# Optimization experiments

Hardware: AMD Instinct MI355X
Metric: run time of the kernel (lower is better)

Reference implementation:

```python
import jax, jax.numpy as jnp
import numpy as np

B, C, H, W = 4, 512, 64, 64
C8 = C // 8
BN_EPS = 1e-5


def setup_inputs() -> dict:
    key = jax.random.key(0)
    ks = jax.random.split(key, 9)
    x = jax.random.normal(ks[0], (B, C, H, W), jnp.float32)
    # 1x1 convs are channel-mixing matrices (out_ch, in_ch), no bias
    wq = 0.02 * jax.random.normal(ks[1], (C8, C), jnp.float32)
    wk = 0.02 * jax.random.normal(ks[2], (C8, C), jnp.float32)
    wv = 0.02 * jax.random.normal(ks[3], (C, C), jnp.float32)
    w_fuse = 0.02 * jax.random.normal(ks[4], (C, C), jnp.float32)
    # gammas init to 0 in the module; use small random values so the
    # attention branches actually contribute to outputs/grads
    gamma_pa = 0.5 + 0.1 * jax.random.normal(ks[5], (1,), jnp.float32)
    gamma_ca = 0.5 + 0.1 * jax.random.normal(ks[6], (1,), jnp.float32)
    bn_scale = 1.0 + 0.1 * jax.random.normal(ks[7], (C,), jnp.float32)
    bn_bias = 0.1 * jax.random.normal(ks[8], (C,), jnp.float32)
    return {"x": x, "wq": wq, "wk": wk, "wv": wv, "w_fuse": w_fuse,
            "gamma_pa": gamma_pa, "gamma_ca": gamma_ca,
            "bn_scale": bn_scale, "bn_bias": bn_bias}


def reference(x, wq, wk, wv, w_fuse, gamma_pa, gamma_ca, bn_scale, bn_bias):
    b, c, h, w = x.shape
    n = h * w
    xf = x.reshape(b, c, n)                         # [B, C, N]

    # ---- Position attention (over N = H*W spatial positions) ----
    q = jnp.einsum('oc,bcn->bon', wq, xf)           # [B, C/8, N]
    k = jnp.einsum('oc,bcn->bon', wk, xf)           # [B, C/8, N]
    v = jnp.einsum('oc,bcn->bon', wv, xf)           # [B, C, N]
    energy = jnp.einsum('bcn,bcm->bnm', q, k)       # [B, N, N] (no scaling, as in source)
    attn = jax.nn.softmax(energy, axis=-1)
    # out = v @ attn^T  ->  out[b,c,n] = sum_m v[b,c,m] * attn[b,n,m]
    pa = jnp.einsum('bcm,bnm->bcn', v, attn).reshape(b, c, h, w)
    pa = gamma_pa * pa + x

    # ---- Channel attention (over C channels, max-subtracted variant) ----
    ce = jnp.einsum('bcn,bdn->bcd', xf, xf)         # [B, C, C]
    ce = jnp.max(ce, axis=-1, keepdims=True) - ce
    cattn = jax.nn.softmax(ce, axis=-1)
    ca = jnp.einsum('bcd,bdn->bcn', cattn, xf).reshape(b, c, h, w)
    ca = gamma_ca * ca + x

    # ---- Fuse: 1x1 conv -> BatchNorm (training-mode batch stats) -> ReLU ----
    s = pa + ca
    y = jnp.einsum('oc,bchw->bohw', w_fuse, s)
    mean = jnp.mean(y, axis=(0, 2, 3), keepdims=True)
    var = jnp.var(y, axis=(0, 2, 3), keepdims=True)
    y = (y - mean) * jax.lax.rsqrt(var + BN_EPS)
    y = y * bn_scale.reshape(1, -1, 1, 1) + bn_bias.reshape(1, -1, 1, 1)
    return jax.nn.relu(y)
```

## Files before the change

### kernel.cpp

```cpp
#include <hip/hip_runtime.h>
#include <cstdint>
#include <cstddef>

#define B_   4
#define C_   512
#define N_   4096
#define BN_EPS 1e-5f

typedef __attribute__((ext_vector_type(8))) short short8;
typedef __attribute__((ext_vector_type(8))) unsigned short ushort8;
typedef __attribute__((ext_vector_type(4))) unsigned short us4_t;
typedef __attribute__((ext_vector_type(4))) float f32x4;

__device__ __forceinline__ unsigned short f2b(float f) {
  union { float f; unsigned u; } v; v.f = f;
  unsigned u = v.u;
  return (unsigned short)((u + 0x7fffu + ((u >> 16) & 1u)) >> 16);
}
__device__ __forceinline__ float b2f(unsigned short h) {
  union { unsigned u; float f; } v; v.u = ((unsigned)h) << 16;
  return v.f;
}
__device__ __forceinline__ void async16(const void* g, void* l) {
  __builtin_amdgcn_global_load_lds((const __attribute__((address_space(1))) void*)g,
                                   (__attribute__((address_space(3))) void*)l, 16, 0, 0);
}


__global__ __launch_bounds__(256) void convert_x_k(const float* __restrict__ x,
                                                   unsigned short* __restrict__ xcn,
                                                   unsigned short* __restrict__ xnc) {
  __shared__ float tile[64][65];
  int c0 = blockIdx.x * 64, n0 = blockIdx.y * 64, b = blockIdx.z;
  const float* xb = x + ((size_t)b * C_ + c0) * N_ + n0;
  unsigned short* cn = xcn + ((size_t)b * C_ + c0) * N_ + n0;
#pragma unroll
  for (int j = 0; j < 16; ++j) {
    int lin = j * 256 + threadIdx.x;
    int rr = lin >> 6, cc = lin & 63;
    float v = xb[(size_t)rr * N_ + cc];
    cn[(size_t)rr * N_ + cc] = f2b(v);
    tile[cc][rr] = v;
  }
  __syncthreads();
  unsigned short* nc = xnc + ((size_t)b * N_ + n0) * C_ + c0;
#pragma unroll
  for (int j = 0; j < 16; ++j) {
    int lin = j * 256 + threadIdx.x;
    int rr = lin >> 6, cc = lin & 63;
    nc[(size_t)rr * C_ + cc] = f2b(tile[rr][cc]);
  }
}

__global__ __launch_bounds__(256) void convert_w_k(const float* __restrict__ wq, const float* __restrict__ wk,
                                                   const float* __restrict__ wv, const float* __restrict__ wf,
                                                   unsigned short* __restrict__ wqk,
                                                   unsigned short* __restrict__ wvb,
                                                   unsigned short* __restrict__ wfb) {
  int i = blockIdx.x * 256 + threadIdx.x;
  if (i < 128 * 512) {
    int row = i >> 9, col = i & 511;
    float v = (row < 64) ? wq[row * 512 + col] : wk[(row - 64) * 512 + col];
    wqk[i] = f2b(v);
  }
  wvb[i] = f2b(wv[i]);
  wfb[i] = f2b(wf[i]);
}


enum { EPI_BF16 = 0, EPI_F32 = 1 };

template<int EPI, bool SPLITK = false>
__global__ __launch_bounds__(256)
void gemm_bt(const unsigned short* __restrict__ A, size_t lda, size_t sA,
             const unsigned short* __restrict__ Bm, size_t ldb, size_t sB,
             void* __restrict__ Cv, size_t ldc, size_t sCbytes, int K) {
  const int bz = blockIdx.z;
  const int m0 = blockIdx.x * 128, n0 = blockIdx.y * 128;
  char* Cb;
  if (SPLITK) {
    int bidx = bz & 3, ch = bz >> 2;
    A  += (size_t)bidx * sA + (size_t)ch * (size_t)K;
    Bm += (size_t)bidx * sB + (size_t)ch * (size_t)K;
    Cb = (char*)Cv + (size_t)bidx * sCbytes + (size_t)ch * 4u * sCbytes;
  } else {
    A  += (size_t)bz * sA;
    Bm += (size_t)bz * sB;
    Cb = (char*)Cv + (size_t)bz * sCbytes;
  }
  __shared__ unsigned short lsA[128 * 32];
  __shared__ unsigned short lsB[128 * 32];
  const int tid = threadIdx.x, lane = tid & 63, w = tid >> 6;
  const int wm = (w >> 1) * 64, wn = (w & 1) * 64;
  const int fr = lane & 15, fk = (lane >> 4) * 8;
  f32x4 acc[4][4];
#pragma unroll
  for (int i = 0; i < 4; ++i)
#pragma unroll
    for (int j = 0; j < 4; ++j) acc[i][j] = (f32x4){0.f, 0.f, 0.f, 0.f};

  const int i0 = tid, i1 = tid + 256;
  for (int k0 = 0; k0 < K; k0 += 32) {
    async16(A  + (size_t)(m0 + (i0 >> 2)) * lda + k0 + (i0 & 3) * 8, (char*)lsA + i0 * 16);
    async16(A  + (size_t)(m0 + (i1 >> 2)) * lda + k0 + (i1 & 3) * 8, (char*)lsA + i1 * 16);
    async16(Bm + (size_t)(n0 + (i0 >> 2)) * ldb + k0 + (i0 & 3) * 8, (char*)lsB + i0 * 16);
    async16(Bm + (size_t)(n0 + (i1 >> 2)) * ldb + k0 + (i1 & 3) * 8, (char*)lsB + i1 * 16);
    __syncthreads();
    short8 af[4], bfr[4];
#pragma unroll
    for (int mi = 0; mi < 4; ++mi)
      af[mi] = *(const short8*)&lsA[(wm + mi * 16 + fr) * 32 + fk];
#pragma unroll
    for (int ni = 0; ni < 4; ++ni)
      bfr[ni] = *(const short8*)&lsB[(wn + ni * 16 + fr) * 32 + fk];
#pragma unroll
    for (int mi = 0; mi < 4; ++mi)
#pragma unroll
      for (int ni = 0; ni < 4; ++ni)
        acc[mi][ni] = __builtin_amdgcn_mfma_f32_16x16x32_bf16(af[mi], bfr[ni], acc[mi][ni], 0, 0, 0);
    __syncthreads();
  }
#pragma unroll
  for (int mi = 0; mi < 4; ++mi)
#pragma unroll
    for (int ni = 0; ni < 4; ++ni)
#pragma unroll
      for (int r = 0; r < 4; ++r) {
        int gr = m0 + wm + mi * 16 + (lane >> 4) * 4 + r;
        int gc = n0 + wn + ni * 16 + fr;
        float v = acc[mi][ni][r];
        if (EPI == EPI_BF16) ((unsigned short*)Cb)[(size_t)gr * ldc + gc] = f2b(v);
        else                 ((float*)Cb)[(size_t)gr * ldc + gc] = v;
      }
}

#define QR 128
#define CC 256
#define KT 128

__global__ __launch_bounds__(512, 2)
void fused_pa_k(const unsigned short* __restrict__ qkT,
                const unsigned short* __restrict__ vmat,
                const unsigned short* __restrict__ caT,
                const unsigned short* __restrict__ xnc,
                const float* __restrict__ gpa_p, const float* __restrict__ gca_p,
                unsigned short* __restrict__ sT) {
  __shared__ unsigned short lsQ[QR * 64];
  __shared__ unsigned short lsK[2][KT * 64];
  __shared__ unsigned short lsV[CC * KT];
  __shared__ unsigned short lsP[QR * KT];
  __shared__ float lsL[8][QR];
  __shared__ float invL[QR];

  const int bid = blockIdx.x;
  const int combo = bid & 7;
  const int b = combo >> 1, chalf = combo & 1;
  const int qt = bid >> 3;
  const int n0 = qt * QR, c0 = chalf * CC;

  const int tid = threadIdx.x, lane = tid & 63, w = tid >> 6;
  const int fr = lane & 15, fq = lane >> 4;
  const int wr = w >> 2, wc = w & 3;

  const unsigned short* qk_b = qkT + (size_t)b * N_ * 128;
  const unsigned short* v_b  = vmat + (size_t)b * C_ * N_;

  f32x4 acc[4][4];
#pragma unroll
  for (int i = 0; i < 4; ++i)
#pragma unroll
    for (int j = 0; j < 4; ++j) acc[i][j] = (f32x4){0.f, 0.f, 0.f, 0.f};
  float lsum[8];
#pragma unroll
  for (int f = 0; f < 8; ++f) lsum[f] = 0.f;

#pragma unroll
  for (int j = 0; j < 2; ++j) {
    int idx = j * 512 + tid;
    int r = idx >> 3, g = idx & 7;
    async16(qk_b + (size_t)(n0 + r) * 128 + ((g ^ (r & 7)) << 3), (char*)lsQ + idx * 16);
  }
#pragma unroll
  for (int j = 0; j < 2; ++j) {
    int idx = j * 512 + tid;
    int r = idx >> 3, g = idx & 7;
    async16(qk_b + (size_t)r * 128 + 64 + ((g ^ (r & 7)) << 3), (char*)lsK[0] + idx * 16);
  }
  __syncthreads();

  for (int it = 0; it < N_ / KT; ++it) {
    const int m0 = it * KT;
#pragma unroll
    for (int j = 0; j < 8; ++j) {
      int idx = j * 512 + tid;
      int c = idx >> 4, g = idx & 15;
      async16(v_b + (size_t)(c0 + c) * N_ + m0 + ((g ^ (c & 7)) << 3), (char*)lsV + idx * 16);
    }
    if (it < N_ / KT - 1) {
      unsigned short* dst = lsK[(it + 1) & 1];
#pragma unroll
      for (int j = 0; j < 2; ++j) {
        int idx = j * 512 + tid;
        int r = idx >> 3, g = idx & 7;
        async16(qk_b + (size_t)(m0 + KT + r) * 128 + 64 + ((g ^ (r & 7)) << 3),
                (char*)dst + idx * 16);
      }
    }
    const unsigned short* lk = lsK[it & 1];
    const int ms = w * 16;
    short8 afk[2];
#pragma unroll
    for (int kk = 0; kk < 2; ++kk)
      afk[kk] = *(const short8*)&lk[(ms + fr) * 64 + (((kk * 4 + fq) ^ (fr & 7)) << 3)];
#pragma unroll
    for (int f = 0; f < 8; ++f) {
      f32x4 e = (f32x4){0.f, 0.f, 0.f, 0.f};
#pragma unroll
      for (int kk = 0; kk < 2; ++kk) {
        short8 bq = *(const short8*)&lsQ[(f * 16 + fr) * 64 + (((kk * 4 + fq) ^ (fr & 7)) << 3)];
        e = __builtin_amdgcn_mfma_f32_16x16x32_bf16(afk[kk], bq, e, 0, 0, 0);
      }
      float p0 = __expf(e[0]), p1 = __expf(e[1]), p2 = __expf(e[2]), p3 = __expf(e[3]);
      float part = (p0 + p1) + (p2 + p3);
      part += __shfl_xor(part, 16, 64);
      part += __shfl_xor(part, 32, 64);
      lsum[f] += part;
      int n = f * 16 + fr;
      int mb = ms + fq * 4;
      us4_t pk = { f2b(p0), f2b(p1), f2b(p2), f2b(p3) };
      *(us4_t*)((char*)lsP + n * 256 + ((((mb >> 3) ^ (n & 7)) << 3) + (mb & 7)) * 2) = pk;
    }
    __syncthreads();
#pragma unroll
    for (int kk4 = 0; kk4 < 4; ++kk4) {
      short8 pa[4], vbf[4];
#pragma unroll
      for (int mi = 0; mi < 4; ++mi) {
        int n = wr * 64 + mi * 16 + fr;
        pa[mi] = *(const short8*)((const char*)lsP + n * 256 + (((kk4 * 4 + fq) ^ (n & 7)) << 4));
      }
#pragma unroll
      for (int ni = 0; ni < 4; ++ni) {
        int c = wc * 64 + ni * 16 + fr;
        vbf[ni] = *(const short8*)((const char*)lsV + c * 256 + (((kk4 * 4 + fq) ^ (c & 7)) << 4));
      }
#pragma unroll
      for (int mi = 0; mi < 4; ++mi)
#pragma unroll
        for (int ni = 0; ni < 4; ++ni)
          acc[mi][ni] = __builtin_amdgcn_mfma_f32_16x16x32_bf16(pa[mi], vbf[ni], acc[mi][ni], 0, 0, 0);
    }
    __syncthreads();
  }

  if (lane < 16) {
#pragma unroll
    for (int f = 0; f < 8; ++f) lsL[w][f * 16 + lane] = lsum[f];
  }
  __syncthreads();
  if (tid < QR) {
    float s = 0.f;
#pragma unroll
    for (int ww = 0; ww < 8; ++ww) s += lsL[ww][tid];
    invL[tid] = 1.f / s;
  }
  __syncthreads();

  const float gpa = gpa_p[0], gca = gca_p[0];
#pragma unroll
  for (int mi = 0; mi < 4; ++mi)
#pragma unroll
    for (int ni = 0; ni < 4; ++ni)
#pragma unroll
      for (int r = 0; r < 4; ++r) {
        int nl = wr * 64 + mi * 16 + fq * 4 + r;
        int gn = n0 + nl;
        int gc = c0 + wc * 64 + ni * 16 + fr;
        size_t eo = ((size_t)b * N_ + gn) * C_ + gc;
        float sv = gpa * acc[mi][ni][r] * invL[nl] + gca * b2f(caT[eo]) + 2.f * b2f(xnc[eo]);
        sT[eo] = f2b(sv);
      }
}

__global__ __launch_bounds__(256) void ce_softmax_k(const float* __restrict__ cepart,
                                                    unsigned short* __restrict__ cattn) {
  int wid = threadIdx.x >> 6, lane = threadIdx.x & 63;
  size_t row = (size_t)blockIdx.x * 4 + wid;
  float v[8]; float mn = 3.4e38f;
#pragma unroll
  for (int i = 0; i < 8; ++i) {
    size_t idx = row * C_ + (size_t)(i * 64 + lane);
    float t = cepart[idx] + cepart[idx + 1048576] + cepart[idx + 2097152] + cepart[idx + 3145728];
    v[i] = t; mn = fminf(mn, t);
  }
#pragma unroll
  for (int o = 1; o < 64; o <<= 1) mn = fminf(mn, __shfl_xor(mn, o, 64));
  float s = 0.f, p[8];
#pragma unroll
  for (int i = 0; i < 8; ++i) { p[i] = expf(mn - v[i]); s += p[i]; }
#pragma unroll
  for (int o = 1; o < 64; o <<= 1) s += __shfl_xor(s, o, 64);
  float inv = 1.f / s;
  unsigned short* orow = cattn + row * C_;
#pragma unroll
  for (int i = 0; i < 8; ++i) orow[i * 64 + lane] = f2b(p[i] * inv);
}

__global__ __launch_bounds__(256) void bn_part_k(const unsigned short* __restrict__ yT,
                                                 float* __restrict__ part) {
  int p = blockIdx.x, t = threadIdx.x;
  const unsigned short* base = yT + (size_t)p * 256 * C_;
  float s0 = 0, q0 = 0, s1 = 0, q1 = 0;
  for (int r = 0; r < 256; ++r) {
    float a = b2f(base[(size_t)r * C_ + t]);
    float b = b2f(base[(size_t)r * C_ + t + 256]);
    s0 += a; q0 += a * a; s1 += b; q1 += b * b;
  }
  float* pp = part + (size_t)p * 1024;
  pp[t] = s0; pp[t + 256] = s1; pp[t + 512] = q0; pp[t + 768] = q1;
}

__global__ __launch_bounds__(256) void bn_final_k(const float* __restrict__ part,
                                                  const float* __restrict__ bns,
                                                  const float* __restrict__ bnb,
                                                  float* __restrict__ ab) {
  int t = threadIdx.x;
#pragma unroll
  for (int cc = 0; cc < 2; ++cc) {
    int c = t + cc * 256;
    float s = 0, q = 0;
    for (int p = 0; p < 64; ++p) { s += part[p * 1024 + c]; q += part[p * 1024 + 512 + c]; }
    float mean = s * (1.f / 16384.f);
    float var  = q * (1.f / 16384.f) - mean * mean;
    float istd = rsqrtf(var + BN_EPS);
    float a = bns[c] * istd;
    float b = bnb[c] - mean * a;
    ab[c * 2] = a; ab[c * 2 + 1] = b;
  }
}

__global__ __launch_bounds__(256) void bn_apply_k(const unsigned short* __restrict__ yT,
                                                  const float* __restrict__ ab,
                                                  float* __restrict__ out) {
  __shared__ float tile[64][65];
  int n0 = blockIdx.x * 64, o0 = blockIdx.y * 64, b = blockIdx.z;
  const unsigned short* yb = yT + ((size_t)b * N_ + n0) * C_ + o0;
#pragma unroll
  for (int j = 0; j < 16; ++j) {
    int lin = j * 256 + threadIdx.x;
    int rr = lin >> 6, cc = lin & 63;
    float v = b2f(yb[(size_t)rr * C_ + cc]);
    float a = ab[(o0 + cc) * 2], bb = ab[(o0 + cc) * 2 + 1];
    tile[cc][rr] = fmaxf(v * a + bb, 0.f);
  }
  __syncthreads();
  float* ob = out + ((size_t)b * C_ + o0) * N_ + n0;
#pragma unroll
  for (int j = 0; j < 16; ++j) {
    int lin = j * 256 + threadIdx.x;
    int rr = lin >> 6, cc = lin & 63;
    ob[(size_t)rr * N_ + cc] = tile[rr][cc];
  }
}


extern "C" void kernel_launch(void* const* d_in, const int* in_sizes, int n_in,
                              void* d_out, int out_size, void* d_ws, size_t ws_size,
                              hipStream_t stream) {
  (void)in_sizes; (void)n_in; (void)out_size; (void)ws_size;
  const float* x   = (const float*)d_in[0];
  const float* wq  = (const float*)d_in[1];
  const float* wk  = (const float*)d_in[2];
  const float* wv  = (const float*)d_in[3];
  const float* wf  = (const float*)d_in[4];
  const float* gpa = (const float*)d_in[5];
  const float* gca = (const float*)d_in[6];
  const float* bns = (const float*)d_in[7];
  const float* bnb = (const float*)d_in[8];
  float* out = (float*)d_out;

  char* ws = (char*)d_ws;
  size_t off = 0;
  auto carve = [&](size_t bytes) -> char* {
    off = (off + 255) & ~(size_t)255;
    char* p = ws + off; off += bytes; return p;
  };

  unsigned short* xcn   = (unsigned short*)carve((size_t)B_ * C_ * N_ * 2);
  unsigned short* xnc   = (unsigned short*)carve((size_t)B_ * C_ * N_ * 2);
  unsigned short* wqkb  = (unsigned short*)carve(128 * 512 * 2);
  unsigned short* wvb   = (unsigned short*)carve(512 * 512 * 2);
  unsigned short* wfb   = (unsigned short*)carve(512 * 512 * 2);
  unsigned short* qkT   = (unsigned short*)carve((size_t)B_ * N_ * 128 * 2);
  unsigned short* vmat  = (unsigned short*)carve((size_t)B_ * C_ * N_ * 2);
  float*          cepart= (float*)carve((size_t)4 * B_ * 512 * 512 * 4);
  unsigned short* cattn = (unsigned short*)carve((size_t)B_ * 512 * 512 * 2);
  unsigned short* caT   = (unsigned short*)carve((size_t)B_ * N_ * C_ * 2);
  float*          bnpart= (float*)carve((size_t)64 * 1024 * 4);
  float*          abv   = (float*)carve(512 * 2 * 4);

  unsigned short* yT = (unsigned short*)cepart;
  unsigned short* sT = xcn;

  convert_x_k<<<dim3(C_ / 64, N_ / 64, B_), 256, 0, stream>>>(x, xcn, xnc);
  convert_w_k<<<dim3(1024), 256, 0, stream>>>(wq, wk, wv, wf, wqkb, wvb, wfb);

  gemm_bt<EPI_BF16><<<dim3(32, 1, 4), 256, 0, stream>>>(
      xnc, 512, (size_t)N_ * C_, wqkb, 512, 0,
      qkT, 128, (size_t)N_ * 128 * 2, 512);

  gemm_bt<EPI_BF16><<<dim3(4, 32, 4), 256, 0, stream>>>(
      wvb, 512, 0, xnc, 512, (size_t)N_ * C_,
      vmat, N_, (size_t)C_ * N_ * 2, 512);

  gemm_bt<EPI_F32, true><<<dim3(4, 4, 16), 256, 0, stream>>>(
      xcn, N_, (size_t)C_ * N_, xcn, N_, (size_t)C_ * N_,
      cepart, 512, (size_t)512 * 512 * 4, 1024);

  ce_softmax_k<<<dim3(B_ * 512 / 4), 256, 0, stream>>>(cepart, cattn);

  gemm_bt<EPI_BF16><<<dim3(32, 4, 4), 256, 0, stream>>>(
      xnc, 512, (size_t)N_ * C_, cattn, 512, (size_t)512 * 512,
      caT, 512, (size_t)N_ * C_ * 2, 512);

  fused_pa_k<<<dim3(256), 512, 0, stream>>>(qkT, vmat, caT, xnc, gpa, gca, sT);

  gemm_bt<EPI_BF16><<<dim3(32, 4, 4), 256, 0, stream>>>(
      sT, 512, (size_t)N_ * C_, wfb, 512, 0,
      yT, 512, (size_t)N_ * C_ * 2, 512);

  bn_part_k<<<dim3(64), 256, 0, stream>>>(yT, bnpart);
  bn_final_k<<<dim3(1), 256, 0, stream>>>(bnpart, bns, bnb, abv);
  bn_apply_k<<<dim3(N_ / 64, C_ / 64, B_), 256, 0, stream>>>(yT, abv, out);
}
```

Baseline: 257.6 us.

## Fuse BN statistics into fuse GEMM, merge weight conversion, retile energy loop

The weight-conversion kernel is folded into the x-conversion launch as an extra z-slice, and the separate BN partial-sum kernel is removed. Per-column sums and squared sums are now computed in the epilogue of the fuse GEMM. The position-attention energy/exp stage is re-tiled so each wave covers 32 keys by 64 queries instead of 16 by 128. This cuts K-fragment reloads and halves the per-wave row sums. Together these remove two launches and a full re-read of yT, at the cost of extra shuffles and LDS traffic in the GEMM epilogue.

```diff
diff --git a/kernel.cpp b/kernel.cpp
--- a/kernel.cpp
+++ b/kernel.cpp
@@ -29,9 +29,28 @@
 
 __global__ __launch_bounds__(256) void convert_x_k(const float* __restrict__ x,
                                                    unsigned short* __restrict__ xcn,
-                                                   unsigned short* __restrict__ xnc) {
+                                                   unsigned short* __restrict__ xnc,
+                                                   const float* __restrict__ wq,
+                                                   const float* __restrict__ wk,
+                                                   const float* __restrict__ wv,
+                                                   const float* __restrict__ wf,
+                                                   unsigned short* __restrict__ wqk,
+                                                   unsigned short* __restrict__ wvb,
+                                                   unsigned short* __restrict__ wfb) {
   __shared__ float tile[64][65];
-  int c0 = blockIdx.x * 64, n0 = blockIdx.y * 64, b = blockIdx.z;
+  int bz = blockIdx.z;
+  if (bz == 4) {
+    int lin = (blockIdx.y * 8 + blockIdx.x) * 256 + threadIdx.x;
+    wvb[lin] = f2b(wv[lin]);  wvb[lin + 131072] = f2b(wv[lin + 131072]);
+    wfb[lin] = f2b(wf[lin]);  wfb[lin + 131072] = f2b(wf[lin + 131072]);
+    if (lin < 65536) {
+      int row = lin >> 9, col = lin & 511;
+      float v = (row < 64) ? wq[row * 512 + col] : wk[(row - 64) * 512 + col];
+      wqk[lin] = f2b(v);
+    }
+    return;
+  }
+  int c0 = blockIdx.x * 64, n0 = blockIdx.y * 64, b = bz;
   const float* xb = x + ((size_t)b * C_ + c0) * N_ + n0;
   unsigned short* cn = xcn + ((size_t)b * C_ + c0) * N_ + n0;
 #pragma unroll
@@ -52,29 +71,15 @@
   }
 }
 
-__global__ __launch_bounds__(256) void convert_w_k(const float* __restrict__ wq, const float* __restrict__ wk,
-                                                   const float* __restrict__ wv, const float* __restrict__ wf,
-                                                   unsigned short* __restrict__ wqk,
-                                                   unsigned short* __restrict__ wvb,
-                                                   unsigned short* __restrict__ wfb) {
-  int i = blockIdx.x * 256 + threadIdx.x;
-  if (i < 128 * 512) {
-    int row = i >> 9, col = i & 511;
-    float v = (row < 64) ? wq[row * 512 + col] : wk[(row - 64) * 512 + col];
-    wqk[i] = f2b(v);
-  }
-  wvb[i] = f2b(wv[i]);
-  wfb[i] = f2b(wf[i]);
-}
-
-
-enum { EPI_BF16 = 0, EPI_F32 = 1 };
+
+enum { EPI_BF16 = 0, EPI_F32 = 1, EPI_YB = 2 };
 
 template<int EPI, bool SPLITK = false>
 __global__ __launch_bounds__(256)
 void gemm_bt(const unsigned short* __restrict__ A, size_t lda, size_t sA,
              const unsigned short* __restrict__ Bm, size_t ldb, size_t sB,
-             void* __restrict__ Cv, size_t ldc, size_t sCbytes, int K) {
+             void* __restrict__ Cv, size_t ldc, size_t sCbytes, int K,
+             float* __restrict__ part) {
   const int bz = blockIdx.z;
   const int m0 = blockIdx.x * 128, n0 = blockIdx.y * 128;
   char* Cb;
@@ -120,6 +125,7 @@
         acc[mi][ni] = __builtin_amdgcn_mfma_f32_16x16x32_bf16(af[mi], bfr[ni], acc[mi][ni], 0, 0, 0);
     __syncthreads();
   }
+  float cs[4] = {0.f, 0.f, 0.f, 0.f}, cq[4] = {0.f, 0.f, 0.f, 0.f};
 #pragma unroll
   for (int mi = 0; mi < 4; ++mi)
 #pragma unroll
@@ -129,9 +135,35 @@
         int gr = m0 + wm + mi * 16 + (lane >> 4) * 4 + r;
         int gc = n0 + wn + ni * 16 + fr;
         float v = acc[mi][ni][r];
-        if (EPI == EPI_BF16) ((unsigned short*)Cb)[(size_t)gr * ldc + gc] = f2b(v);
-        else                 ((float*)Cb)[(size_t)gr * ldc + gc] = v;
-      }
+        if (EPI == EPI_F32) ((float*)Cb)[(size_t)gr * ldc + gc] = v;
+        else                ((unsigned short*)Cb)[(size_t)gr * ldc + gc] = f2b(v);
+        if (EPI == EPI_YB) { cs[ni] += v; cq[ni] += v * v; }
+      }
+  if (EPI == EPI_YB) {
+#pragma unroll
+    for (int ni = 0; ni < 4; ++ni) {
+      cs[ni] += __shfl_xor(cs[ni], 16, 64); cs[ni] += __shfl_xor(cs[ni], 32, 64);
+      cq[ni] += __shfl_xor(cq[ni], 16, 64); cq[ni] += __shfl_xor(cq[ni], 32, 64);
+    }
+    float* fb = (float*)lsA;
+    if (lane < 16) {
+#pragma unroll
+      for (int ni = 0; ni < 4; ++ni) {
+        int col = wn + ni * 16 + lane;
+        fb[((w >> 1) * 128 + col) * 2]     = cs[ni];
+        fb[((w >> 1) * 128 + col) * 2 + 1] = cq[ni];
+      }
+    }
+    __syncthreads();
+    if (tid < 128) {
+      float s = fb[tid * 2] + fb[(128 + tid) * 2];
+      float q = fb[tid * 2 + 1] + fb[(128 + tid) * 2 + 1];
+      int rg = bz * 32 + blockIdx.x;
+      int gcol = blockIdx.y * 128 + tid;
+      part[(size_t)rg * 1024 + gcol * 2]     = s;
+      part[(size_t)rg * 1024 + gcol * 2 + 1] = q;
+    }
+  }
 }
 
 #define QR 128
@@ -149,7 +181,7 @@
   __shared__ unsigned short lsK[2][KT * 64];
   __shared__ unsigned short lsV[CC * KT];
   __shared__ unsigned short lsP[QR * KT];
-  __shared__ float lsL[8][QR];
+  __shared__ float lsL[8][64];
   __shared__ float invL[QR];
 
   const int bid = blockIdx.x;
@@ -161,6 +193,8 @@
   const int tid = threadIdx.x, lane = tid & 63, w = tid >> 6;
   const int fr = lane & 15, fq = lane >> 4;
   const int wr = w >> 2, wc = w & 3;
+  const int ms = (w & 3) * 32;
+  const int nb = (w >> 2) * 64;
 
   const unsigned short* qk_b = qkT + (size_t)b * N_ * 128;
   const unsigned short* v_b  = vmat + (size_t)b * C_ * N_;
@@ -170,9 +204,7 @@
   for (int i = 0; i < 4; ++i)
 #pragma unroll
     for (int j = 0; j < 4; ++j) acc[i][j] = (f32x4){0.f, 0.f, 0.f, 0.f};
-  float lsum[8];
-#pragma unroll
-  for (int f = 0; f < 8; ++f) lsum[f] = 0.f;
+  float lsum[4] = {0.f, 0.f, 0.f, 0.f};
 
 #pragma unroll
   for (int j = 0; j < 2; ++j) {
@@ -207,28 +239,32 @@
       }
     }
     const unsigned short* lk = lsK[it & 1];
-    const int ms = w * 16;
-    short8 afk[2];
-#pragma unroll
-    for (int kk = 0; kk < 2; ++kk)
-      afk[kk] = *(const short8*)&lk[(ms + fr) * 64 + (((kk * 4 + fq) ^ (fr & 7)) << 3)];
-#pragma unroll
-    for (int f = 0; f < 8; ++f) {
-      f32x4 e = (f32x4){0.f, 0.f, 0.f, 0.f};
-#pragma unroll
-      for (int kk = 0; kk < 2; ++kk) {
-        short8 bq = *(const short8*)&lsQ[(f * 16 + fr) * 64 + (((kk * 4 + fq) ^ (fr & 7)) << 3)];
-        e = __builtin_amdgcn_mfma_f32_16x16x32_bf16(afk[kk], bq, e, 0, 0, 0);
-      }
-      float p0 = __expf(e[0]), p1 = __expf(e[1]), p2 = __expf(e[2]), p3 = __expf(e[3]);
-      float part = (p0 + p1) + (p2 + p3);
+    short8 afk[2][2];
+#pragma unroll
+    for (int mi = 0; mi < 2; ++mi)
+#pragma unroll
+      for (int kk = 0; kk < 2; ++kk)
+        afk[mi][kk] = *(const short8*)&lk[(ms + mi * 16 + fr) * 64 + (((kk * 4 + fq) ^ (fr & 7)) << 3)];
+#pragma unroll
+    for (int f = 0; f < 4; ++f) {
+      int n = nb + f * 16 + fr;
+      short8 bq0 = *(const short8*)&lsQ[n * 64 + (((0 * 4 + fq) ^ (fr & 7)) << 3)];
+      short8 bq1 = *(const short8*)&lsQ[n * 64 + (((1 * 4 + fq) ^ (fr & 7)) << 3)];
+      float part = 0.f;
+#pragma unroll
+      for (int mi = 0; mi < 2; ++mi) {
+        f32x4 e = (f32x4){0.f, 0.f, 0.f, 0.f};
+        e = __builtin_amdgcn_mfma_f32_16x16x32_bf16(afk[mi][0], bq0, e, 0, 0, 0);
+        e = __builtin_amdgcn_mfma_f32_16x16x32_bf16(afk[mi][1], bq1, e, 0, 0, 0);
+        float p0 = __expf(e[0]), p1 = __expf(e[1]), p2 = __expf(e[2]), p3 = __expf(e[3]);
+        part += (p0 + p1) + (p2 + p3);
+        int mb = ms + mi * 16 + fq * 4;
+        us4_t pk = { f2b(p0), f2b(p1), f2b(p2), f2b(p3) };
+        *(us4_t*)((char*)lsP + n * 256 + ((((mb >> 3) ^ (n & 7)) << 3) + (mb & 7)) * 2) = pk;
+      }
       part += __shfl_xor(part, 16, 64);
       part += __shfl_xor(part, 32, 64);
       lsum[f] += part;
-      int n = f * 16 + fr;
-      int mb = ms + fq * 4;
-      us4_t pk = { f2b(p0), f2b(p1), f2b(p2), f2b(p3) };
-      *(us4_t*)((char*)lsP + n * 256 + ((((mb >> 3) ^ (n & 7)) << 3) + (mb & 7)) * 2) = pk;
     }
     __syncthreads();
 #pragma unroll
@@ -255,14 +291,12 @@
 
   if (lane < 16) {
 #pragma unroll
-    for (int f = 0; f < 8; ++f) lsL[w][f * 16 + lane] = lsum[f];
+    for (int f = 0; f < 4; ++f) lsL[w][f * 16 + lane] = lsum[f];
   }
   __syncthreads();
   if (tid < QR) {
-    float s = 0.f;
-#pragma unroll
-    for (int ww = 0; ww < 8; ++ww) s += lsL[ww][tid];
-    invL[tid] = 1.f / s;
+    int nh = tid >> 6, j = tid & 63;
+    invL[tid] = 1.f / (lsL[4 * nh][j] + lsL[4 * nh + 1][j] + lsL[4 * nh + 2][j] + lsL[4 * nh + 3][j]);
   }
   __syncthreads();
 
@@ -306,20 +340,6 @@
   for (int i = 0; i < 8; ++i) orow[i * 64 + lane] = f2b(p[i] * inv);
 }
 
-__global__ __launch_bounds__(256) void bn_part_k(const unsigned short* __restrict__ yT,
-                                                 float* __restrict__ part) {
-  int p = blockIdx.x, t = threadIdx.x;
-  const unsigned short* base = yT + (size_t)p * 256 * C_;
-  float s0 = 0, q0 = 0, s1 = 0, q1 = 0;
-  for (int r = 0; r < 256; ++r) {
-    float a = b2f(base[(size_t)r * C_ + t]);
-    float b = b2f(base[(size_t)r * C_ + t + 256]);
-    s0 += a; q0 += a * a; s1 += b; q1 += b * b;
-  }
-  float* pp = part + (size_t)p * 1024;
-  pp[t] = s0; pp[t + 256] = s1; pp[t + 512] = q0; pp[t + 768] = q1;
-}
-
 __global__ __launch_bounds__(256) void bn_final_k(const float* __restrict__ part,
                                                   const float* __restrict__ bns,
                                                   const float* __restrict__ bnb,
@@ -329,7 +349,7 @@
   for (int cc = 0; cc < 2; ++cc) {
     int c = t + cc * 256;
     float s = 0, q = 0;
-    for (int p = 0; p < 64; ++p) { s += part[p * 1024 + c]; q += part[p * 1024 + 512 + c]; }
+    for (int p = 0; p < 128; ++p) { s += part[(size_t)p * 1024 + c * 2]; q += part[(size_t)p * 1024 + c * 2 + 1]; }
     float mean = s * (1.f / 16384.f);
     float var  = q * (1.f / 16384.f) - mean * mean;
     float istd = rsqrtf(var + BN_EPS);
@@ -396,40 +416,39 @@
   float*          cepart= (float*)carve((size_t)4 * B_ * 512 * 512 * 4);
   unsigned short* cattn = (unsigned short*)carve((size_t)B_ * 512 * 512 * 2);
   unsigned short* caT   = (unsigned short*)carve((size_t)B_ * N_ * C_ * 2);
-  float*          bnpart= (float*)carve((size_t)64 * 1024 * 4);
+  float*          bnpart= (float*)carve((size_t)128 * 1024 * 4);
   float*          abv   = (float*)carve(512 * 2 * 4);
 
   unsigned short* yT = (unsigned short*)cepart;
   unsigned short* sT = xcn;
 
-  convert_x_k<<<dim3(C_ / 64, N_ / 64, B_), 256, 0, stream>>>(x, xcn, xnc);
-  convert_w_k<<<dim3(1024), 256, 0, stream>>>(wq, wk, wv, wf, wqkb, wvb, wfb);
+  convert_x_k<<<dim3(C_ / 64, N_ / 64, 5), 256, 0, stream>>>(
+      x, xcn, xnc, wq, wk, wv, wf, wqkb, wvb, wfb);
 
   gemm_bt<EPI_BF16><<<dim3(32, 1, 4), 256, 0, stream>>>(
       xnc, 512, (size_t)N_ * C_, wqkb, 512, 0,
-      qkT, 128, (size_t)N_ * 128 * 2, 512);
+      qkT, 128, (size_t)N_ * 128 * 2, 512, nullptr);
 
   gemm_bt<EPI_BF16><<<dim3(4, 32, 4), 256, 0, stream>>>(
       wvb, 512, 0, xnc, 512, (size_t)N_ * C_,
-      vmat, N_, (size_t)C_ * N_ * 2, 512);
+      vmat, N_, (size_t)C_ * N_ * 2, 512, nullptr);
 
   gemm_bt<EPI_F32, true><<<dim3(4, 4, 16), 256, 0, stream>>>(
       xcn, N_, (size_t)C_ * N_, xcn, N_, (size_t)C_ * N_,
-      cepart, 512, (size_t)512 * 512 * 4, 1024);
+      cepart, 512, (size_t)512 * 512 * 4, 1024, nullptr);
 
   ce_softmax_k<<<dim3(B_ * 512 / 4), 256, 0, stream>>>(cepart, cattn);
 
   gemm_bt<EPI_BF16><<<dim3(32, 4, 4), 256, 0, stream>>>(
       xnc, 512, (size_t)N_ * C_, cattn, 512, (size_t)512 * 512,
-      caT, 512, (size_t)N_ * C_ * 2, 512);
+      caT, 512, (size_t)N_ * C_ * 2, 512, nullptr);
 
   fused_pa_k<<<dim3(256), 512, 0, stream>>>(qkT, vmat, caT, xnc, gpa, gca, sT);
 
-  gemm_bt<EPI_BF16><<<dim3(32, 4, 4), 256, 0, stream>>>(
+  gemm_bt<EPI_YB><<<dim3(32, 4, 4), 256, 0, stream>>>(
       sT, 512, (size_t)N_ * C_, wfb, 512, 0,
-      yT, 512, (size_t)N_ * C_ * 2, 512);
-
-  bn_part_k<<<dim3(64), 256, 0, stream>>>(yT, bnpart);
+      yT, 512, (size_t)N_ * C_ * 2, 512, bnpart);
+
   bn_final_k<<<dim3(1), 256, 0, stream>>>(bnpart, bns, bnb, abv);
   bn_apply_k<<<dim3(N_ / 64, C_ / 64, B_), 256, 0, stream>>>(yT, abv, out);
 }
```

Measured after the change: 242.4 us. 1.06x faster.
